# Kernel tuning notes

Measured on AMD Instinct MI355X. Metric: run time of the kernel, lower is better.

Reference implementation:

```python
import jax, jax.numpy as jnp
import numpy as np

N = 100_000      # nodes
E = 1_600_000    # edges
C_IN = 3         # pos dim
C = 128          # inter_dim == oup_dim
EPS = 1e-5       # BatchNorm eps


def setup_inputs() -> dict:
    key = jax.random.key(0)
    ks = iter(jax.random.split(key, 64))
    inp = {}
    inp['pos'] = jax.random.normal(next(ks), (N, C_IN), dtype=jnp.float32)
    inp['edge_index'] = jax.random.randint(next(ks), (2, E), 0, N, dtype=jnp.int32)
    dims = [C_IN, C, C, C, C]
    for i in range(1, 5):
        cin, cout = dims[i - 1], dims[i]
        inp[f'wl{i}'] = jax.random.normal(next(ks), (cin, cout), jnp.float32) * 0.05
        inp[f'bl{i}'] = jnp.zeros((cout,), jnp.float32)
        inp[f'wr{i}'] = jax.random.normal(next(ks), (cin, cout), jnp.float32) * 0.05
        inp[f'g{i}'] = jax.random.uniform(next(ks), (cout,), jnp.float32, 0.5, 1.5)
        inp[f'be{i}'] = jax.random.normal(next(ks), (cout,), jnp.float32) * 0.1
        inp[f'm{i}'] = jax.random.normal(next(ks), (cout,), jnp.float32) * 0.1
        inp[f'v{i}'] = jax.random.uniform(next(ks), (cout,), jnp.float32, 0.5, 1.5)
    for j, (cin, cout) in enumerate([(C, C), (C, C), (C, C)], start=1):
        inp[f'wf{j}'] = jax.random.normal(next(ks), (cin, cout), jnp.float32) * 0.05
        inp[f'bf{j}'] = jnp.zeros((cout,), jnp.float32)
    return inp


def _sage(x, src, dst, wl, bl, wr):
    # PyG SAGEConv: lin_l(mean_{j->i} x_j) + lin_r(x_i)
    msg_sum = jax.ops.segment_sum(x[src], dst, num_segments=N)          # [N, Cin]
    deg = jax.ops.segment_sum(jnp.ones((src.shape[0], 1), x.dtype), dst, num_segments=N)
    agg = msg_sum / jnp.maximum(deg, 1.0)
    return agg @ wl + bl + x @ wr


def _bn(x, g, b, m, v):
    return g * (x - m) * jax.lax.rsqrt(v + EPS) + b


def reference(pos, edge_index,
              wl1, bl1, wr1, g1, be1, m1, v1,
              wl2, bl2, wr2, g2, be2, m2, v2,
              wl3, bl3, wr3, g3, be3, m3, v3,
              wl4, bl4, wr4, g4, be4, m4, v4,
              wf1, bf1, wf2, bf2, wf3, bf3):
    src, dst = edge_index[0], edge_index[1]
    layers = [(wl1, bl1, wr1, g1, be1, m1, v1),
              (wl2, bl2, wr2, g2, be2, m2, v2),
              (wl3, bl3, wr3, g3, be3, m3, v3),
              (wl4, bl4, wr4, g4, be4, m4, v4)]
    x = pos
    for (wl, bl, wr, g, b, m, v) in layers:
        x = jax.nn.relu(_bn(_sage(x, src, dst, wl, bl, wr), g, b, m, v))
        # dropout p=0.1 inactive at inference
    x = x @ wf1 + bf1
    x = jax.nn.relu(x) @ wf2 + bf2
    x = x @ wf3 + bf3
    return x  # cls=False: raw output, no log_softmax
```

## Files before the change

### kernel.cpp

```cpp
#include <hip/hip_runtime.h>

#define NN 100000
#define EE 1600000
#define CC 128
#define NP 100032
#define NBK 782
#define BCAP 2304

typedef _Float16 f16;
typedef __attribute__((ext_vector_type(2))) f16 f16x2;
typedef __attribute__((ext_vector_type(8))) f16 f16x8;
typedef __attribute__((ext_vector_type(4))) float f32x4;

#define MFMA16(a, b, c) __builtin_amdgcn_mfma_f32_16x16x32_f16(a, b, c, 0, 0, 0)

__global__ __launch_bounds__(1024) void k_part(const int* __restrict__ src,
                                               const int* __restrict__ dst,
                                               int* __restrict__ bcur,
                                               unsigned* __restrict__ bedge) {
  __shared__ int hist[NBK];
  __shared__ int base[NBK];
  const int t = threadIdx.x;
  for (int i = t; i < NBK; i += 1024) hist[i] = 0;
  __syncthreads();
  const int4* src4 = (const int4*)src;
  const int4* dst4 = (const int4*)dst;
  int4 s[4], d[4];
  bool val[4];
#pragma unroll
  for (int w = 0; w < 4; w++) {
    int i4 = blockIdx.x * 4096 + w * 1024 + t;
    val[w] = (i4 < EE / 4);
    if (val[w]) {
      s[w] = src4[i4];
      d[w] = dst4[i4];
      atomicAdd(&hist[d[w].x >> 7], 1);
      atomicAdd(&hist[d[w].y >> 7], 1);
      atomicAdd(&hist[d[w].z >> 7], 1);
      atomicAdd(&hist[d[w].w >> 7], 1);
    }
  }
  __syncthreads();
  for (int i = t; i < NBK; i += 1024) {
    int c = hist[i];
    base[i] = c ? atomicAdd(&bcur[i], c) : 0;
  }
  __syncthreads();
  for (int i = t; i < NBK; i += 1024) hist[i] = 0;
  __syncthreads();
#pragma unroll
  for (int w = 0; w < 4; w++) {
    if (val[w]) {
      int ss[4] = {s[w].x, s[w].y, s[w].z, s[w].w};
      int dd[4] = {d[w].x, d[w].y, d[w].z, d[w].w};
#pragma unroll
      for (int q = 0; q < 4; q++) {
        int b = dd[q] >> 7;
        int p = atomicAdd(&hist[b], 1);
        int slot = base[b] + p;
        if (slot < BCAP)
          bedge[(size_t)b * BCAP + slot] =
              (unsigned)ss[q] | ((unsigned)(dd[q] & 127) << 17);
      }
    }
  }
}

__global__ __launch_bounds__(256) void k_bdeg(const int* __restrict__ bcur,
                                              const unsigned* __restrict__ bedge,
                                              int* __restrict__ degi) {
  __shared__ int h[128];
  const int b = blockIdx.x;
  const int t = threadIdx.x;
  if (t < 128) h[t] = 0;
  __syncthreads();
  const int cnt = min(bcur[b], BCAP);
  const unsigned* be = bedge + (size_t)b * BCAP;
  for (int i = t; i < cnt; i += 256) atomicAdd(&h[(be[i] >> 17) & 127], 1);
  __syncthreads();
  int n = b * 128 + t;
  if (t < 128 && n < NN) degi[n] = h[t];
}

__global__ __launch_bounds__(1024) void k_scan1(const int* __restrict__ degi,
                                                int* __restrict__ bsum) {
  __shared__ int sh[1024];
  int t = threadIdx.x;
  int i = blockIdx.x * 1024 + t;
  sh[t] = (i < NN) ? degi[i] : 0;
  __syncthreads();
  for (int d = 512; d > 0; d >>= 1) {
    if (t < d) sh[t] += sh[t + d];
    __syncthreads();
  }
  if (t == 0) bsum[blockIdx.x] = sh[0];
}

__global__ __launch_bounds__(128) void k_scan2(const int* __restrict__ bsum,
                                               int* __restrict__ bbase,
                                               int* __restrict__ off) {
  __shared__ int sh[128];
  int t = threadIdx.x;
  int v = (t < 98) ? bsum[t] : 0;
  sh[t] = v;
  __syncthreads();
  for (int d = 1; d < 128; d <<= 1) {
    int a = (t >= d) ? sh[t - d] : 0;
    __syncthreads();
    sh[t] += a;
    __syncthreads();
  }
  if (t < 98) bbase[t] = sh[t] - v;
  if (t == 127) off[NN] = sh[127];
}

__global__ __launch_bounds__(1024) void k_scan3(const int* __restrict__ degi,
                                                const int* __restrict__ bbase,
                                                int* __restrict__ off) {
  __shared__ int sh[1024];
  int t = threadIdx.x;
  int i = blockIdx.x * 1024 + t;
  int v = (i < NN) ? degi[i] : 0;
  sh[t] = v;
  __syncthreads();
  for (int d = 1; d < 1024; d <<= 1) {
    int a = (t >= d) ? sh[t - d] : 0;
    __syncthreads();
    sh[t] += a;
    __syncthreads();
  }
  if (i < NN) off[i] = bbase[blockIdx.x] + sh[t] - v;
}

__global__ __launch_bounds__(256) void k_bfill(const int* __restrict__ bcur,
                                               const unsigned* __restrict__ bedge,
                                               const int* __restrict__ off,
                                               int* __restrict__ csr) {
  __shared__ int curs[128];
  __shared__ int offs[128];
  const int b = blockIdx.x;
  const int t = threadIdx.x;
  if (t < 128) {
    int n = b * 128 + t;
    offs[t] = (n < NN) ? off[n] : 0;
    curs[t] = 0;
  }
  __syncthreads();
  const int cnt = min(bcur[b], BCAP);
  const unsigned* be = bedge + (size_t)b * BCAP;
  for (int i = t; i < cnt; i += 256) {
    unsigned u = be[i];
    int node = (u >> 17) & 127;
    int sv = u & 0x1FFFF;
    int p = atomicAdd(&curs[node], 1);
    csr[offs[node] + p] = sv;
  }
}

struct WPtrs { const float* w[9]; };
__global__ __launch_bounds__(256) void k_packw(WPtrs wp, f16* __restrict__ out) {
  int t = blockIdx.x * 256 + threadIdx.x;
  int mat = t >> 14;
  int idx = t & 16383;
  int j = idx & 7;
  int lane = (idx >> 3) & 63;
  int ks = (idx >> 9) & 3;
  int nt = idx >> 11;
  int c16 = lane & 15, quad = lane >> 4;
  int k = ks * 32 + quad * 8 + j;
  int n = nt * 16 + c16;
  out[(size_t)mat * 16384 + idx] = (f16)wp.w[mat][k * CC + n];
}

__global__ __launch_bounds__(256) void k_agg3(const int* __restrict__ off,
                                              const int* __restrict__ csr,
                                              const float* __restrict__ pos,
                                              float* __restrict__ agg3) {
  int n = blockIdx.x * 256 + threadIdx.x;
  if (n >= NN) return;
  int b = off[n], e = off[n + 1];
  float a0 = 0.f, a1 = 0.f, a2 = 0.f;
  for (int i = b; i < e; i++) {
    int s = csr[i];
    a0 += pos[s * 3 + 0];
    a1 += pos[s * 3 + 1];
    a2 += pos[s * 3 + 2];
  }
  float rd = 1.0f / fmaxf((float)(e - b), 1.0f);
  agg3[n * 3 + 0] = a0 * rd;
  agg3[n * 3 + 1] = a1 * rd;
  agg3[n * 3 + 2] = a2 * rd;
}

__global__ __launch_bounds__(128) void k_node1(
    const float* __restrict__ agg3, const float* __restrict__ pos,
    const float* __restrict__ wl, const float* __restrict__ bl,
    const float* __restrict__ wr, const float* __restrict__ g,
    const float* __restrict__ be, const float* __restrict__ bm,
    const float* __restrict__ bv, f16* __restrict__ x) {
  int n = blockIdx.x;
  int c = threadIdx.x;
  __shared__ float sa[3], sp[3];
  if (c < 3) {
    sa[c] = agg3[n * 3 + c];
    sp[c] = pos[n * 3 + c];
  }
  __syncthreads();
  float acc = bl[c];
#pragma unroll
  for (int k = 0; k < 3; k++) {
    acc += sa[k] * wl[k * CC + c];
    acc += sp[k] * wr[k * CC + c];
  }
  float sc = g[c] * rsqrtf(bv[c] + 1e-5f);
  float yv = fmaxf((acc - bm[c]) * sc + be[c], 0.0f);
  x[(size_t)n * CC + c] = (f16)yv;
}

__global__ __launch_bounds__(256) void k_aggregate(const int* __restrict__ off,
                                                   const int* __restrict__ csr,
                                                   const f16* __restrict__ x,
                                                   f16* __restrict__ agg) {
  const int n = blockIdx.x * 4 + (threadIdx.x >> 6);
  const int lane = threadIdx.x & 63;
  const int b = off[n], e = off[n + 1];
  float a0 = 0.f, a1 = 0.f;
  int i = b;
  for (; i + 4 <= e; i += 4) {
    int s0 = csr[i], s1 = csr[i + 1], s2 = csr[i + 2], s3 = csr[i + 3];
    f16x2 v0 = *(const f16x2*)(x + (size_t)s0 * CC + lane * 2);
    f16x2 v1 = *(const f16x2*)(x + (size_t)s1 * CC + lane * 2);
    f16x2 v2 = *(const f16x2*)(x + (size_t)s2 * CC + lane * 2);
    f16x2 v3 = *(const f16x2*)(x + (size_t)s3 * CC + lane * 2);
    a0 += ((float)v0[0] + (float)v1[0]) + ((float)v2[0] + (float)v3[0]);
    a1 += ((float)v0[1] + (float)v1[1]) + ((float)v2[1] + (float)v3[1]);
  }
  for (; i < e; i++) {
    int s = csr[i];
    f16x2 v = *(const f16x2*)(x + (size_t)s * CC + lane * 2);
    a0 += (float)v[0];
    a1 += (float)v[1];
  }
  const float rd = 1.0f / fmaxf((float)(e - b), 1.0f);
  f16x2 o;
  o[0] = (f16)(a0 * rd);
  o[1] = (f16)(a1 * rd);
  *(f16x2*)(agg + (size_t)n * CC + lane * 2) = o;
}

__global__ __launch_bounds__(256) void k_sage_mfma(
    f16* __restrict__ x, const f16* __restrict__ agg,
    const f16* __restrict__ wl, const f16* __restrict__ wr,
    const float* __restrict__ bl, const float* __restrict__ g,
    const float* __restrict__ be, const float* __restrict__ bm,
    const float* __restrict__ bv) {
  const int lane = threadIdx.x & 63;
  const int wave = threadIdx.x >> 6;
  const int c16 = lane & 15;
  const int quad = lane >> 4;
  const int n0 = blockIdx.x * 64 + wave * 16;
  const int rowX = n0 + c16;
  const int rowA = min(rowX, NN - 1);
  const f16* px = x + (size_t)rowX * CC + quad * 8;
  const f16* pa = agg + (size_t)rowA * CC + quad * 8;
  f32x4 acc[8];
#pragma unroll
  for (int t = 0; t < 8; t++) acc[t] = {0.f, 0.f, 0.f, 0.f};
#pragma unroll
  for (int ks = 0; ks < 4; ks++) {
    f16x8 Ax = *(const f16x8*)(px + ks * 32);
    f16x8 Aa = *(const f16x8*)(pa + ks * 32);
#pragma unroll
    for (int nt = 0; nt < 8; nt++) {
      const size_t wo = (size_t)((nt * 4 + ks) * 64 + lane) * 8;
      f16x8 Bl = *(const f16x8*)(wl + wo);
      f16x8 Br = *(const f16x8*)(wr + wo);
      acc[nt] = MFMA16(Aa, Bl, acc[nt]);
      acc[nt] = MFMA16(Ax, Br, acc[nt]);
    }
  }
#pragma unroll
  for (int nt = 0; nt < 8; nt++) {
    const int col = nt * 16 + c16;
    const float blc = bl[col];
    const float sc = g[col] * rsqrtf(bv[col] + 1e-5f);
    const float mm = bm[col];
    const float bb = be[col];
#pragma unroll
    for (int r = 0; r < 4; r++) {
      const int node = n0 + quad * 4 + r;
      if (node < NN) {
        float yv = fmaxf((acc[nt][r] + blc - mm) * sc + bb, 0.0f);
        x[(size_t)node * CC + col] = (f16)yv;
      }
    }
  }
}

__global__ __launch_bounds__(256) void k_dense_fused(
    const f16* __restrict__ x, const f16* __restrict__ w1,
    const f16* __restrict__ w2, const f16* __restrict__ w3,
    const float* __restrict__ b1, const float* __restrict__ b2,
    const float* __restrict__ b3, float* __restrict__ out) {
  const int lane = threadIdx.x & 63;
  const int wave = threadIdx.x >> 6;
  const int c16 = lane & 15;
  const int quad = lane >> 4;
  const int n0 = blockIdx.x * 64 + wave * 16;
  const int lrow = wave * 16;
  __shared__ f16 sh[64][136];

  f32x4 acc[8];
#pragma unroll
  for (int t = 0; t < 8; t++) acc[t] = {0.f, 0.f, 0.f, 0.f};
  const f16* px = x + (size_t)(n0 + c16) * CC + quad * 8;
#pragma unroll
  for (int ks = 0; ks < 4; ks++) {
    f16x8 Ax = *(const f16x8*)(px + ks * 32);
#pragma unroll
    for (int nt = 0; nt < 8; nt++) {
      f16x8 B = *(const f16x8*)(w1 + (size_t)((nt * 4 + ks) * 64 + lane) * 8);
      acc[nt] = MFMA16(Ax, B, acc[nt]);
    }
  }
#pragma unroll
  for (int nt = 0; nt < 8; nt++) {
    const int col = nt * 16 + c16;
    const float bc = b1[col];
#pragma unroll
    for (int r = 0; r < 4; r++)
      sh[lrow + quad * 4 + r][col] = (f16)fmaxf(acc[nt][r] + bc, 0.0f);
  }
  __syncthreads();
#pragma unroll
  for (int t = 0; t < 8; t++) acc[t] = {0.f, 0.f, 0.f, 0.f};
#pragma unroll
  for (int ks = 0; ks < 4; ks++) {
    f16x8 Ax = *(const f16x8*)&sh[lrow + c16][ks * 32 + quad * 8];
#pragma unroll
    for (int nt = 0; nt < 8; nt++) {
      f16x8 B = *(const f16x8*)(w2 + (size_t)((nt * 4 + ks) * 64 + lane) * 8);
      acc[nt] = MFMA16(Ax, B, acc[nt]);
    }
  }
  __syncthreads();
#pragma unroll
  for (int nt = 0; nt < 8; nt++) {
    const int col = nt * 16 + c16;
    const float bc = b2[col];
#pragma unroll
    for (int r = 0; r < 4; r++)
      sh[lrow + quad * 4 + r][col] = (f16)(acc[nt][r] + bc);
  }
  __syncthreads();
#pragma unroll
  for (int t = 0; t < 8; t++) acc[t] = {0.f, 0.f, 0.f, 0.f};
#pragma unroll
  for (int ks = 0; ks < 4; ks++) {
    f16x8 Ax = *(const f16x8*)&sh[lrow + c16][ks * 32 + quad * 8];
#pragma unroll
    for (int nt = 0; nt < 8; nt++) {
      f16x8 B = *(const f16x8*)(w3 + (size_t)((nt * 4 + ks) * 64 + lane) * 8);
      acc[nt] = MFMA16(Ax, B, acc[nt]);
    }
  }
#pragma unroll
  for (int nt = 0; nt < 8; nt++) {
    const int col = nt * 16 + c16;
    const float bc = b3[col];
#pragma unroll
    for (int r = 0; r < 4; r++) {
      const int node = n0 + quad * 4 + r;
      if (node < NN) out[(size_t)node * CC + col] = acc[nt][r] + bc;
    }
  }
}

extern "C" void kernel_launch(void* const* d_in, const int* in_sizes, int n_in,
                              void* d_out, int out_size, void* d_ws,
                              size_t ws_size, hipStream_t stream) {
  const float* pos = (const float*)d_in[0];
  const int* ei = (const int*)d_in[1];
  const int* src = ei;
  const int* dst = ei + EE;
  auto P = [&](int i) { return (const float*)d_in[i]; };

  int* bcur = (int*)d_ws;
  int* off = bcur + NBK;
  int* degi = off + NN + 2;
  int* bsum = degi + NN;
  int* bbase = bsum + 128;
  unsigned* bedge = (unsigned*)(bbase + 128);
  int* csr = (int*)(bedge + (size_t)NBK * BCAP);
  f16* wp16 = (f16*)(csr + EE);
  f16* x = wp16 + 9 * 16384;

  f16* agg = (f16*)d_out;

  hipMemsetAsync(bcur, 0, NBK * sizeof(int), stream);

  k_part<<<(EE / 4 + 4095) / 4096, 1024, 0, stream>>>(src, dst, bcur, bedge);
  k_bdeg<<<NBK, 256, 0, stream>>>(bcur, bedge, degi);
  const int SB = (NN + 1023) / 1024;
  k_scan1<<<SB, 1024, 0, stream>>>(degi, bsum);
  k_scan2<<<1, 128, 0, stream>>>(bsum, bbase, off);
  k_scan3<<<SB, 1024, 0, stream>>>(degi, bbase, off);
  k_bfill<<<NBK, 256, 0, stream>>>(bcur, bedge, off, csr);

  WPtrs wp;
  const int wsrc[9] = {9, 11, 16, 18, 23, 25, 30, 32, 34};
  for (int i = 0; i < 9; i++) wp.w[i] = P(wsrc[i]);
  k_packw<<<(9 * 16384) / 256, 256, 0, stream>>>(wp, wp16);

  k_agg3<<<(NN + 255) / 256, 256, 0, stream>>>(off, csr, pos, (float*)d_out);
  k_node1<<<NN, 128, 0, stream>>>((const float*)d_out, pos, P(2), P(3), P(4),
                                  P(5), P(6), P(7), P(8), x);

  const int NB = NP / 64;
  for (int l = 1; l < 4; l++) {
    int base = 2 + 7 * l;
    int mat = (l - 1) * 2;
    k_aggregate<<<NN / 4, 256, 0, stream>>>(off, csr, x, agg);
    k_sage_mfma<<<NB, 256, 0, stream>>>(
        x, agg, wp16 + (size_t)mat * 16384, wp16 + (size_t)(mat + 1) * 16384,
        P(base + 1), P(base + 3), P(base + 4), P(base + 5), P(base + 6));
  }

  k_dense_fused<<<NB, 256, 0, stream>>>(x, wp16 + (size_t)6 * 16384,
                                        wp16 + (size_t)7 * 16384,
                                        wp16 + (size_t)8 * 16384, P(31), P(33),
                                        P(35), (float*)d_out);
}
```

Before: 603.3 us.

## Streamline CSR build, unroll gather loop, double-buffer features, drop dense syncs

```diff
diff --git a/kernel.cpp b/kernel.cpp
--- a/kernel.cpp
+++ b/kernel.cpp
@@ -26,6 +26,7 @@
   const int4* src4 = (const int4*)src;
   const int4* dst4 = (const int4*)dst;
   int4 s[4], d[4];
+  int rk[16];
   bool val[4];
 #pragma unroll
   for (int w = 0; w < 4; w++) {
@@ -34,10 +35,10 @@
     if (val[w]) {
       s[w] = src4[i4];
       d[w] = dst4[i4];
-      atomicAdd(&hist[d[w].x >> 7], 1);
-      atomicAdd(&hist[d[w].y >> 7], 1);
-      atomicAdd(&hist[d[w].z >> 7], 1);
-      atomicAdd(&hist[d[w].w >> 7], 1);
+      rk[w * 4 + 0] = atomicAdd(&hist[d[w].x >> 7], 1);
+      rk[w * 4 + 1] = atomicAdd(&hist[d[w].y >> 7], 1);
+      rk[w * 4 + 2] = atomicAdd(&hist[d[w].z >> 7], 1);
+      rk[w * 4 + 3] = atomicAdd(&hist[d[w].w >> 7], 1);
     }
   }
   __syncthreads();
@@ -45,8 +46,6 @@
     int c = hist[i];
     base[i] = c ? atomicAdd(&bcur[i], c) : 0;
   }
-  __syncthreads();
-  for (int i = t; i < NBK; i += 1024) hist[i] = 0;
   __syncthreads();
 #pragma unroll
   for (int w = 0; w < 4; w++) {
@@ -56,8 +55,7 @@
 #pragma unroll
       for (int q = 0; q < 4; q++) {
         int b = dd[q] >> 7;
-        int p = atomicAdd(&hist[b], 1);
-        int slot = base[b] + p;
+        int slot = base[b] + rk[w * 4 + q];
         if (slot < BCAP)
           bedge[(size_t)b * BCAP + slot] =
               (unsigned)ss[q] | ((unsigned)(dd[q] & 127) << 17);
@@ -66,61 +64,12 @@
   }
 }
 
-__global__ __launch_bounds__(256) void k_bdeg(const int* __restrict__ bcur,
-                                              const unsigned* __restrict__ bedge,
-                                              int* __restrict__ degi) {
-  __shared__ int h[128];
-  const int b = blockIdx.x;
-  const int t = threadIdx.x;
-  if (t < 128) h[t] = 0;
-  __syncthreads();
-  const int cnt = min(bcur[b], BCAP);
-  const unsigned* be = bedge + (size_t)b * BCAP;
-  for (int i = t; i < cnt; i += 256) atomicAdd(&h[(be[i] >> 17) & 127], 1);
-  __syncthreads();
-  int n = b * 128 + t;
-  if (t < 128 && n < NN) degi[n] = h[t];
-}
-
-__global__ __launch_bounds__(1024) void k_scan1(const int* __restrict__ degi,
-                                                int* __restrict__ bsum) {
-  __shared__ int sh[1024];
-  int t = threadIdx.x;
-  int i = blockIdx.x * 1024 + t;
-  sh[t] = (i < NN) ? degi[i] : 0;
-  __syncthreads();
-  for (int d = 512; d > 0; d >>= 1) {
-    if (t < d) sh[t] += sh[t + d];
-    __syncthreads();
-  }
-  if (t == 0) bsum[blockIdx.x] = sh[0];
-}
-
-__global__ __launch_bounds__(128) void k_scan2(const int* __restrict__ bsum,
-                                               int* __restrict__ bbase,
-                                               int* __restrict__ off) {
-  __shared__ int sh[128];
-  int t = threadIdx.x;
-  int v = (t < 98) ? bsum[t] : 0;
-  sh[t] = v;
-  __syncthreads();
-  for (int d = 1; d < 128; d <<= 1) {
-    int a = (t >= d) ? sh[t - d] : 0;
-    __syncthreads();
-    sh[t] += a;
-    __syncthreads();
-  }
-  if (t < 98) bbase[t] = sh[t] - v;
-  if (t == 127) off[NN] = sh[127];
-}
-
-__global__ __launch_bounds__(1024) void k_scan3(const int* __restrict__ degi,
-                                                const int* __restrict__ bbase,
+__global__ __launch_bounds__(1024) void k_bscan(const int* __restrict__ bcur,
+                                                int* __restrict__ bbase,
                                                 int* __restrict__ off) {
   __shared__ int sh[1024];
   int t = threadIdx.x;
-  int i = blockIdx.x * 1024 + t;
-  int v = (i < NN) ? degi[i] : 0;
+  int v = (t < NBK) ? min(bcur[t], BCAP) : 0;
   sh[t] = v;
   __syncthreads();
   for (int d = 1; d < 1024; d <<= 1) {
@@ -129,31 +78,47 @@
     sh[t] += a;
     __syncthreads();
   }
-  if (i < NN) off[i] = bbase[blockIdx.x] + sh[t] - v;
-}
-
-__global__ __launch_bounds__(256) void k_bfill(const int* __restrict__ bcur,
-                                               const unsigned* __restrict__ bedge,
-                                               const int* __restrict__ off,
-                                               int* __restrict__ csr) {
+  if (t < NBK) bbase[t] = sh[t] - v;
+  if (t == 1023) off[NN] = sh[1023];
+}
+
+__global__ __launch_bounds__(256) void k_bfill2(const int* __restrict__ bcur,
+                                                const int* __restrict__ bbase,
+                                                const unsigned* __restrict__ bedge,
+                                                int* __restrict__ off,
+                                                int* __restrict__ csr) {
+  __shared__ int h[128];
+  __shared__ int sc[128];
   __shared__ int curs[128];
-  __shared__ int offs[128];
   const int b = blockIdx.x;
   const int t = threadIdx.x;
-  if (t < 128) {
-    int n = b * 128 + t;
-    offs[t] = (n < NN) ? off[n] : 0;
-    curs[t] = 0;
-  }
+  if (t < 128) h[t] = 0;
   __syncthreads();
   const int cnt = min(bcur[b], BCAP);
   const unsigned* be = bedge + (size_t)b * BCAP;
+  for (int i = t; i < cnt; i += 256) atomicAdd(&h[(be[i] >> 17) & 127], 1);
+  __syncthreads();
+  int v = (t < 128) ? h[t] : 0;
+  if (t < 128) sc[t] = v;
+  __syncthreads();
+  for (int d = 1; d < 128; d <<= 1) {
+    int a = (t >= d && t < 128) ? sc[t - d] : 0;
+    __syncthreads();
+    if (t < 128) sc[t] += a;
+    __syncthreads();
+  }
+  if (t < 128) {
+    int o = bbase[b] + sc[t] - v;
+    int n = b * 128 + t;
+    if (n < NN) off[n] = o;
+    curs[t] = o;
+  }
+  __syncthreads();
   for (int i = t; i < cnt; i += 256) {
     unsigned u = be[i];
     int node = (u >> 17) & 127;
-    int sv = u & 0x1FFFF;
     int p = atomicAdd(&curs[node], 1);
-    csr[offs[node] + p] = sv;
+    csr[p] = (int)(u & 0x1FFFF);
   }
 }
 
@@ -226,6 +191,20 @@
   const int b = off[n], e = off[n + 1];
   float a0 = 0.f, a1 = 0.f;
   int i = b;
+  for (; i + 8 <= e; i += 8) {
+    int sdx[8];
+#pragma unroll
+    for (int q = 0; q < 8; q++) sdx[q] = csr[i + q];
+    f16x2 v[8];
+#pragma unroll
+    for (int q = 0; q < 8; q++)
+      v[q] = *(const f16x2*)(x + (size_t)sdx[q] * CC + lane * 2);
+#pragma unroll
+    for (int q = 0; q < 8; q++) {
+      a0 += (float)v[q][0];
+      a1 += (float)v[q][1];
+    }
+  }
   for (; i + 4 <= e; i += 4) {
     int s0 = csr[i], s1 = csr[i + 1], s2 = csr[i + 2], s3 = csr[i + 3];
     f16x2 v0 = *(const f16x2*)(x + (size_t)s0 * CC + lane * 2);
@@ -249,11 +228,11 @@
 }
 
 __global__ __launch_bounds__(256) void k_sage_mfma(
-    f16* __restrict__ x, const f16* __restrict__ agg,
-    const f16* __restrict__ wl, const f16* __restrict__ wr,
-    const float* __restrict__ bl, const float* __restrict__ g,
-    const float* __restrict__ be, const float* __restrict__ bm,
-    const float* __restrict__ bv) {
+    const f16* __restrict__ xin, f16* __restrict__ xout,
+    const f16* __restrict__ agg, const f16* __restrict__ wl,
+    const f16* __restrict__ wr, const float* __restrict__ bl,
+    const float* __restrict__ g, const float* __restrict__ be,
+    const float* __restrict__ bm, const float* __restrict__ bv) {
   const int lane = threadIdx.x & 63;
   const int wave = threadIdx.x >> 6;
   const int c16 = lane & 15;
@@ -261,7 +240,7 @@
   const int n0 = blockIdx.x * 64 + wave * 16;
   const int rowX = n0 + c16;
   const int rowA = min(rowX, NN - 1);
-  const f16* px = x + (size_t)rowX * CC + quad * 8;
+  const f16* px = xin + (size_t)rowX * CC + quad * 8;
   const f16* pa = agg + (size_t)rowA * CC + quad * 8;
   f32x4 acc[8];
 #pragma unroll
@@ -291,7 +270,7 @@
       const int node = n0 + quad * 4 + r;
       if (node < NN) {
         float yv = fmaxf((acc[nt][r] + blc - mm) * sc + bb, 0.0f);
-        x[(size_t)node * CC + col] = (f16)yv;
+        xout[(size_t)node * CC + col] = (f16)yv;
       }
     }
   }
@@ -331,7 +310,6 @@
     for (int r = 0; r < 4; r++)
       sh[lrow + quad * 4 + r][col] = (f16)fmaxf(acc[nt][r] + bc, 0.0f);
   }
-  __syncthreads();
 #pragma unroll
   for (int t = 0; t < 8; t++) acc[t] = {0.f, 0.f, 0.f, 0.f};
 #pragma unroll
@@ -343,7 +321,6 @@
       acc[nt] = MFMA16(Ax, B, acc[nt]);
     }
   }
-  __syncthreads();
 #pragma unroll
   for (int nt = 0; nt < 8; nt++) {
     const int col = nt * 16 + c16;
@@ -352,7 +329,6 @@
     for (int r = 0; r < 4; r++)
       sh[lrow + quad * 4 + r][col] = (f16)(acc[nt][r] + bc);
   }
-  __syncthreads();
 #pragma unroll
   for (int t = 0; t < 8; t++) acc[t] = {0.f, 0.f, 0.f, 0.f};
 #pragma unroll
@@ -386,26 +362,21 @@
   auto P = [&](int i) { return (const float*)d_in[i]; };
 
   int* bcur = (int*)d_ws;
-  int* off = bcur + NBK;
-  int* degi = off + NN + 2;
-  int* bsum = degi + NN;
-  int* bbase = bsum + 128;
-  unsigned* bedge = (unsigned*)(bbase + 128);
+  int* bbase = bcur + NBK;
+  int* off = bbase + NBK;
+  unsigned* bedge = (unsigned*)(off + NN + 2);
   int* csr = (int*)(bedge + (size_t)NBK * BCAP);
   f16* wp16 = (f16*)(csr + EE);
-  f16* x = wp16 + 9 * 16384;
+  f16* xa = wp16 + 9 * 16384;
+  f16* xb = xa + (size_t)NP * CC;
 
   f16* agg = (f16*)d_out;
 
   hipMemsetAsync(bcur, 0, NBK * sizeof(int), stream);
 
   k_part<<<(EE / 4 + 4095) / 4096, 1024, 0, stream>>>(src, dst, bcur, bedge);
-  k_bdeg<<<NBK, 256, 0, stream>>>(bcur, bedge, degi);
-  const int SB = (NN + 1023) / 1024;
-  k_scan1<<<SB, 1024, 0, stream>>>(degi, bsum);
-  k_scan2<<<1, 128, 0, stream>>>(bsum, bbase, off);
-  k_scan3<<<SB, 1024, 0, stream>>>(degi, bbase, off);
-  k_bfill<<<NBK, 256, 0, stream>>>(bcur, bedge, off, csr);
+  k_bscan<<<1, 1024, 0, stream>>>(bcur, bbase, off);
+  k_bfill2<<<NBK, 256, 0, stream>>>(bcur, bbase, bedge, off, csr);
 
   WPtrs wp;
   const int wsrc[9] = {9, 11, 16, 18, 23, 25, 30, 32, 34};
@@ -414,19 +385,26 @@
 
   k_agg3<<<(NN + 255) / 256, 256, 0, stream>>>(off, csr, pos, (float*)d_out);
   k_node1<<<NN, 128, 0, stream>>>((const float*)d_out, pos, P(2), P(3), P(4),
-                                  P(5), P(6), P(7), P(8), x);
+                                  P(5), P(6), P(7), P(8), xa);
 
   const int NB = NP / 64;
+  const f16* xi = xa;
+  f16* xo = xb;
   for (int l = 1; l < 4; l++) {
     int base = 2 + 7 * l;
     int mat = (l - 1) * 2;
-    k_aggregate<<<NN / 4, 256, 0, stream>>>(off, csr, x, agg);
-    k_sage_mfma<<<NB, 256, 0, stream>>>(
-        x, agg, wp16 + (size_t)mat * 16384, wp16 + (size_t)(mat + 1) * 16384,
-        P(base + 1), P(base + 3), P(base + 4), P(base + 5), P(base + 6));
-  }
-
-  k_dense_fused<<<NB, 256, 0, stream>>>(x, wp16 + (size_t)6 * 16384,
+    k_aggregate<<<NN / 4, 256, 0, stream>>>(off, csr, xi, agg);
+    k_sage_mfma<<<NB, 256, 0, stream>>>(xi, xo, agg,
+                                        wp16 + (size_t)mat * 16384,
+                                        wp16 + (size_t)(mat + 1) * 16384,
+                                        P(base + 1), P(base + 3), P(base + 4),
+                                        P(base + 5), P(base + 6));
+    const f16* t = xi;
+    xi = xo;
+    xo = (f16*)t;
+  }
+
+  k_dense_fused<<<NB, 256, 0, stream>>>(xi, wp16 + (size_t)6 * 16384,
                                         wp16 + (size_t)7 * 16384,
                                         wp16 + (size_t)8 * 16384, P(31), P(33),
                                         P(35), (float*)d_out);
```

Result: faster. 584.8 us (-3.1%).
